# Optimization experiments

Hardware: AMD Instinct MI355X
Metric: run time of the kernel (lower is better)

## Reference

```python
import jax, jax.numpy as jnp
import numpy as np

N, C, H, W = 16, 64, 256, 256


def setup_inputs() -> dict:
    key = jax.random.key(0)
    ks = jax.random.split(key, 7)
    s = 1.0 / np.sqrt(C)
    return {
        "h": jax.random.normal(ks[0], (N, C, H, W), dtype=jnp.float32),
        "wq": jax.random.normal(ks[1], (C, C), dtype=jnp.float32) * s,
        "bq": jax.random.normal(ks[2], (C,), dtype=jnp.float32) * 0.01,
        "wk": jax.random.normal(ks[3], (C, C), dtype=jnp.float32) * s,
        "bk": jax.random.normal(ks[4], (C,), dtype=jnp.float32) * 0.01,
        "wv": jax.random.normal(ks[5], (C, C), dtype=jnp.float32) * s,
        "bv": jax.random.normal(ks[6], (C,), dtype=jnp.float32) * 0.01,
    }


def _proj(h, w, b):
    # 1x1 conv == per-pixel channel linear: (N,C,H,W) x (Cout,Cin)
    return jnp.einsum("nchw,oc->nohw", h, w) + b[None, :, None, None]


def reference(h, wq, bq, wk, bk, wv, bv):
    q = _proj(h, wq, bq)
    k = _proj(h, wk, bk)
    v = _proj(h, wv, bv)

    # NOTE: original code uses n = k.shape[-1] of the UNPERMUTED k => n = W
    scale = 1.0 / jnp.sqrt(jnp.asarray(W, dtype=q.dtype))

    # Channel-wise ROW attention: permute (N,C,H,W)->(N,W,H,C), attend over H
    attn_r = jnp.einsum("nchw,ngw->nwhg", q, jnp.einsum("ncgw->ngw" if False else "ncgw->ncgw", k)[0] if False else jnp.einsum("ncgw->ncgw", k).sum(axis=0) * 0) if False else None
    # row: q_r (n,w,h,c) @ k_r^T (n,w,c,g) -> (n,w,h,g)
    scores_r = jnp.einsum("nchw,ncgw->nwhg", q, k) * scale
    p_r = jax.nn.softmax(scores_r, axis=-1)
    out_r = jnp.einsum("nwhg,ncgw->nchw", p_r, v)  # back to (N,C,H,W)

    # Channel-wise COLUMN attention: permute (N,C,H,W)->(N,H,W,C), attend over W
    scores_c = jnp.einsum("nchw,nchu->nhwu", q, k) * scale
    p_c = jax.nn.softmax(scores_c, axis=-1)
    out_c = jnp.einsum("nhwu,nchu->nchw", p_c, v)

    attention = out_r + out_c
    return attention + h
```

## Files before the change

### kernel.cpp

```cpp
#include <hip/hip_runtime.h>


typedef unsigned short u16t;
typedef __bf16 bf16x8 __attribute__((ext_vector_type(8)));
typedef __bf16 bf16x2 __attribute__((ext_vector_type(2)));
typedef float  f32x4  __attribute__((ext_vector_type(4)));
typedef u16t   us8    __attribute__((ext_vector_type(8)));
typedef u16t   us4    __attribute__((ext_vector_type(4)));
typedef unsigned uu4  __attribute__((ext_vector_type(4)));

#define DEVINL __device__ __forceinline__

#define SCL16 0.09016844f

DEVINL u16t f2bf(float f){
    return __builtin_bit_cast(u16t, (__bf16)f);
}
DEVINL float bf2f(u16t h){
    unsigned u = ((unsigned)h) << 16;
    return __builtin_bit_cast(float, u);
}
DEVINL unsigned pk2(float lo, float hi){
    bf16x2 t; t[0] = (__bf16)lo; t[1] = (__bf16)hi;
    return __builtin_bit_cast(unsigned, t);
}
DEVINL f32x4 mfma16(bf16x8 a, bf16x8 b, f32x4 c){
    return __builtin_amdgcn_mfma_f32_16x16x32_bf16(a, b, c, 0, 0, 0);
}
DEVINL int xswz(int row, int chunk){
    return row*128 + ((chunk << 4) ^ (((row & 7) ^ ((row >> 2) & 7)) << 4));
}

__global__ __launch_bounds__(256) void transpose_kernel(const float* __restrict__ h,
                                                        u16t* __restrict__ hT){
    __shared__ float tile[64][257];
    const int bid = blockIdx.x;
    const int n = bid >> 8, y = bid & 255;
    const int tid = threadIdx.x;
    {
        const int c = tid >> 2, w0 = (tid & 3) * 64;
        const int base = ((n * 64 + c) * 256 + y) * 256 + w0;
        #pragma unroll
        for (int i = 0; i < 16; ++i){
            f32x4 v = *(const f32x4*)(h + base + i * 4);
            tile[c][w0 + i*4 + 0] = v[0];
            tile[c][w0 + i*4 + 1] = v[1];
            tile[c][w0 + i*4 + 2] = v[2];
            tile[c][w0 + i*4 + 3] = v[3];
        }
    }
    __syncthreads();
    #pragma unroll
    for (int j = 0; j < 4; ++j){
        const int task = tid + 256 * j;
        const int w = task >> 2, c0 = (task & 3) * 16;
        us8 o0, o1;
        #pragma unroll
        for (int e = 0; e < 8; ++e) o0[e] = f2bf(tile[c0 + e][w]);
        #pragma unroll
        for (int e = 0; e < 8; ++e) o1[e] = f2bf(tile[c0 + 8 + e][w]);
        const int ob = ((n * 256 + y) * 256 + w) * 64 + c0;
        *(us8*)(hT + ob)     = o0;
        *(us8*)(hT + ob + 8) = o1;
    }
}

template<int COL>
__global__ __launch_bounds__(512, 4) void attn_kernel(
    const u16t* __restrict__ Xg,
    const float* __restrict__ wq, const float* __restrict__ bq,
    const float* __restrict__ wk, const float* __restrict__ wvw,
    const float* __restrict__ bvp,
    u16t* __restrict__ Og,
    float* __restrict__ outp)
{
    __shared__ __align__(16) u16t Xs[16384];
    __shared__ __align__(16) u16t VtF[16384];
    __shared__ __align__(16) u16t AtF[4096];
    __shared__ __align__(16) float w16s[256];
    __shared__ float wkbqs[64];
    __shared__ float bvs[64];

    const int tid  = threadIdx.x;
    const int lane = tid & 63;
    const int wv   = tid >> 6;
    const int bid  = blockIdx.x;
    const int n    = bid >> 8;
    const int idx  = bid & 255;
    const int l15  = lane & 15;
    const int l4   = lane >> 4;
    const int nbase = n * 4194304;
    const int sbase = nbase + idx * 16384;
    const int aa   = l15 >> 2, bb = l15 & 3;
    const char* Xc = (const char*)Xs;

    {
        const int r0 = tid >> 3, cc = tid & 7;
        const int swzS = (((r0 & 7) ^ ((tid >> 5) & 7)) << 4);
        char* pdst = (char*)Xs + r0*128 + ((cc << 4) ^ swzS);
        const u16t* psrc = Xg + (COL ? (sbase + r0*64 + cc*8)
                                     : (nbase + r0*16384 + idx*64 + cc*8));
        const int gstep = COL ? 4096 : 1048576;
        #pragma unroll
        for (int pass = 0; pass < 4; ++pass){
            us8 v = *(const us8*)(psrc + pass*gstep);
            *(us8*)(pdst + pass*8192) = v;
        }
    }

    {
        const int mtA = wv >> 1;
        us8 aku[2];
        #pragma unroll
        for (int kt = 0; kt < 2; ++kt)
            #pragma unroll
            for (int e = 0; e < 8; ++e)
                aku[kt][e] = f2bf(wk[(kt*32 + l4*8 + e)*64 + mtA*16 + l15]);
        #pragma unroll
        for (int t2 = 0; t2 < 2; ++t2){
            const int ntA = (2*wv + t2) & 3;
            us8 bqu[2];
            #pragma unroll
            for (int kt = 0; kt < 2; ++kt)
                #pragma unroll
                for (int e = 0; e < 8; ++e)
                    bqu[kt][e] = f2bf(wq[(kt*32 + l4*8 + e)*64 + ntA*16 + l15]);
            f32x4 acc = {0.f,0.f,0.f,0.f};
            acc = mfma16(__builtin_bit_cast(bf16x8, aku[0]), __builtin_bit_cast(bf16x8, bqu[0]), acc);
            acc = mfma16(__builtin_bit_cast(bf16x8, aku[1]), __builtin_bit_cast(bf16x8, bqu[1]), acc);
            #pragma unroll
            for (int r = 0; r < 4; ++r){
                const int cp = mtA*16 + 4*l4 + r;
                const int cc = ntA*16 + l15;
                const int vtq  = 2*(cp>>5) + ((cp>>2)&1);
                const int mrow = 4*((cp>>3)&3) + (cp&3);
                const int f    = vtq*2 + (cc>>5);
                AtF[(f*64 + ((cc>>3)&3)*16 + mrow)*8 + (cc&7)] = f2bf(acc[r] * SCL16);
            }
        }
    }
    if (tid < 64){
        float acc = 0.f;
        for (int o = 0; o < 64; ++o) acc += wk[o*64 + tid] * bq[o];
        wkbqs[tid] = acc;
        bvs[tid] = bvp[tid];
    }
    __syncthreads();

    {
        const int ct = wv >> 1;
        bf16x8 awv[2];
        #pragma unroll
        for (int ktc = 0; ktc < 2; ++ktc){
            const float* wp = wvw + (ct*16 + l15)*64 + ktc*32 + l4*8;
            f32x4 v0 = *(const f32x4*)wp;
            f32x4 v1 = *(const f32x4*)(wp + 4);
            us8 u;
            #pragma unroll
            for (int e = 0; e < 4; ++e){ u[e] = f2bf(v0[e]); u[4+e] = f2bf(v1[e]); }
            awv[ktc] = __builtin_bit_cast(bf16x8, u);
        }
        const char* pb0 = Xc + (wv&1)*16384 + l15*128;
        const int swzE = (((l15&7) ^ aa) << 4);
        const int swzO = (((l15&7) ^ (4+aa)) << 4);
        const int cE0 = (l4<<4) ^ swzE, cE1 = ((4+l4)<<4) ^ swzE;
        const int cO0 = (l4<<4) ^ swzO, cO1 = ((4+l4)<<4) ^ swzO;
        char* pvw = (char*)VtF + (ct*8 + (wv&1)*4)*1024 + (l15>>3)*256 + l4*64 + (l15&7)*2;
        #pragma unroll
        for (int t = 0; t < 8; ++t){
            const int o0 = (t&1) ? cO0 : cE0, o1 = (t&1) ? cO1 : cE1;
            bf16x8 bx0 = *(const bf16x8*)(pb0 + t*2048 + o0);
            bf16x8 bx1 = *(const bf16x8*)(pb0 + t*2048 + o1);
            f32x4 z = {0.f,0.f,0.f,0.f};
            z = mfma16(awv[0], bx0, z);
            z = mfma16(awv[1], bx1, z);
            char* pw8 = pvw + (t>>1)*1024 + (t&1)*512;
            #pragma unroll
            for (int rr = 0; rr < 4; ++rr)
                *(u16t*)(pw8 + rr*16) = f2bf(z[rr]);
        }
    }
    if (tid < 256){
        float acc = 0.f;
        #pragma unroll
        for (int cc = 0; cc < 8; ++cc){
            us8 xv = *(const us8*)(Xc + xswz(tid, cc));
            #pragma unroll
            for (int e = 0; e < 8; ++e) acc += bf2f(xv[e]) * wkbqs[cc*8 + e];
        }
        w16s[tid] = acc * SCL16;
    }
    __syncthreads();

    const int rowoff = 8*aa + bb;

    const char* pat = (const char*)AtF + lane*16;
    bf16x8 xq[2][2];
    #pragma unroll
    for (int mi = 0; mi < 2; ++mi){
        const int mt = wv + 8*mi;
        xq[mi][0] = *(const bf16x8*)(Xc + xswz(mt*16 + l15, l4));
        xq[mi][1] = *(const bf16x8*)(Xc + xswz(mt*16 + l15, 4 + l4));
    }
    uu4 qp[2][2];
    #pragma unroll
    for (int vtq = 0; vtq < 4; ++vtq){
        bf16x8 a0 = *(const bf16x8*)(pat + (vtq*2 + 0)*1024);
        bf16x8 a1 = *(const bf16x8*)(pat + (vtq*2 + 1)*1024);
        #pragma unroll
        for (int mi = 0; mi < 2; ++mi){
            f32x4 z = {0.f,0.f,0.f,0.f};
            z = mfma16(a0, xq[mi][0], z);
            z = mfma16(a1, xq[mi][1], z);
            qp[mi][vtq>>1][(vtq&1)*2 + 0] = pk2(z[0], z[1]);
            qp[mi][vtq>>1][(vtq&1)*2 + 1] = pk2(z[2], z[3]);
        }
    }
    bf16x8 qb[2][2];
    qb[0][0] = __builtin_bit_cast(bf16x8, qp[0][0]);
    qb[0][1] = __builtin_bit_cast(bf16x8, qp[0][1]);
    qb[1][0] = __builtin_bit_cast(bf16x8, qp[1][0]);
    qb[1][1] = __builtin_bit_cast(bf16x8, qp[1][1]);

    const int swz0 = (bb ^ (2*aa)) << 4;
    const int swz1 = ((4 + bb) ^ ((2*aa + 1) & 7)) << 4;
    const char* pv00 = Xc + rowoff*128 + ((l4<<4) ^ swz0);
    const char* pv01 = Xc + rowoff*128 + (((4+l4)<<4) ^ swz0);
    const char* pv10 = Xc + rowoff*128 + 512 + ((l4<<4) ^ swz1);
    const char* pv11 = Xc + rowoff*128 + 512 + (((4+l4)<<4) ^ swz1);
    const char* pvv = (const char*)VtF + lane*16;
    const char* pw  = (const char*)w16s + l4*32;

    uu4 onep; onep[0] = 0x3F803F80u; onep[1] = 0x3F803F80u; onep[2] = 0x3F803F80u; onep[3] = 0x3F803F80u;
    const bf16x8 onesb = __builtin_bit_cast(bf16x8, onep);

    f32x4 po[2][4] = {{{0.f,0.f,0.f,0.f},{0.f,0.f,0.f,0.f},{0.f,0.f,0.f,0.f},{0.f,0.f,0.f,0.f}},
                      {{0.f,0.f,0.f,0.f},{0.f,0.f,0.f,0.f},{0.f,0.f,0.f,0.f},{0.f,0.f,0.f,0.f}}};
    f32x4 po_sum[2] = {{0.f,0.f,0.f,0.f},{0.f,0.f,0.f,0.f}};

    #pragma unroll
    for (int kt = 0; kt < 8; ++kt){
        bf16x8 xa00 = *(const bf16x8*)(pv00 + kt*4096);
        bf16x8 xa01 = *(const bf16x8*)(pv01 + kt*4096);
        bf16x8 xa10 = *(const bf16x8*)(pv10 + kt*4096);
        bf16x8 xa11 = *(const bf16x8*)(pv11 + kt*4096);
        f32x4 cw0 = *(const f32x4*)(pw + kt*128);
        f32x4 cw1 = *(const f32x4*)(pw + kt*128 + 16);
        bf16x8 vb[4];
        #pragma unroll
        for (int nt = 0; nt < 4; ++nt)
            vb[nt] = *(const bf16x8*)(pvv + (nt*8 + kt)*1024);

        __builtin_amdgcn_s_setprio(1);
        bf16x8 pa[2];
        #pragma unroll
        for (int mi = 0; mi < 2; ++mi){
            uu4 tt;
            f32x4 z0 = cw0;
            z0 = mfma16(xa00, qb[mi][0], z0);
            z0 = mfma16(xa01, qb[mi][1], z0);
            tt[0] = pk2(__builtin_amdgcn_exp2f(z0[0]), __builtin_amdgcn_exp2f(z0[1]));
            tt[1] = pk2(__builtin_amdgcn_exp2f(z0[2]), __builtin_amdgcn_exp2f(z0[3]));
            f32x4 z1 = cw1;
            z1 = mfma16(xa10, qb[mi][0], z1);
            z1 = mfma16(xa11, qb[mi][1], z1);
            tt[2] = pk2(__builtin_amdgcn_exp2f(z1[0]), __builtin_amdgcn_exp2f(z1[1]));
            tt[3] = pk2(__builtin_amdgcn_exp2f(z1[2]), __builtin_amdgcn_exp2f(z1[3]));
            pa[mi] = __builtin_bit_cast(bf16x8, tt);
            po_sum[mi] = mfma16(pa[mi], onesb, po_sum[mi]);
        }
        #pragma unroll
        for (int nt = 0; nt < 4; ++nt){
            po[0][nt] = mfma16(pa[0], vb[nt], po[0][nt]);
            po[1][nt] = mfma16(pa[1], vb[nt], po[1][nt]);
        }
        __builtin_amdgcn_s_setprio(0);
    }

    __syncthreads();
    u16t* OutS = VtF;

    if (!COL){
        #pragma unroll
        for (int mi = 0; mi < 2; ++mi){
            const int mt = wv + 8*mi;
            float rs[4];
            #pragma unroll
            for (int r = 0; r < 4; ++r) rs[r] = __builtin_amdgcn_rcpf(po_sum[mi][r]);
            #pragma unroll
            for (int nt = 0; nt < 4; ++nt){
                const int c = nt*16 + l15;
                const float b = bvs[c];
                #pragma unroll
                for (int r01 = 0; r01 < 2; ++r01){
                    float vr[2];
                    #pragma unroll
                    for (int e = 0; e < 2; ++e){
                        const int r = 2*r01 + e;
                        const int y = mt*16 + 4*l4 + r;
                        const float xres = bf2f(*(const u16t*)(Xc + xswz(y, c>>3) + (c&7)*2));
                        vr[e] = po[mi][nt][r]*rs[r] + b + xres;
                    }
                    const int y0 = mt*16 + 4*l4 + 2*r01;
                    const unsigned v = pk2(vr[0], vr[1]);
                    *(u16t*)((char*)OutS + y0*128 + (((c>>3)<<4) ^ ((y0&7)<<4)) + (c&7)*2) = (u16t)v;
                    *(u16t*)((char*)OutS + (y0+1)*128 + (((c>>3)<<4) ^ (((y0+1)&7)<<4)) + (c&7)*2) = (u16t)(v >> 16);
                }
            }
        }
        __syncthreads();
        #pragma unroll
        for (int p = 0; p < 4; ++p){
            const int id = p*512 + tid;
            const int y = id >> 3, ch = id & 7;
            us8 v = *(const us8*)((const char*)OutS + y*128 + ((ch<<4) ^ ((y&7)<<4)));
            *(us8*)(Og + sbase + y*64 + ch*8) = v;
        }
    } else {
        #pragma unroll
        for (int p = 0; p < 4; ++p){
            const int id = p*512 + tid;
            const int wl = id >> 3, ch = id & 7;
            us8 v = *(const us8*)(Og + nbase + wl*16384 + idx*64 + ch*8);
            *(us8*)(Xs + id*8) = v;
        }
        __syncthreads();
        #pragma unroll
        for (int mi = 0; mi < 2; ++mi){
            const int mt = wv + 8*mi;
            float rs[4];
            #pragma unroll
            for (int r = 0; r < 4; ++r) rs[r] = __builtin_amdgcn_rcpf(po_sum[mi][r]);
            #pragma unroll
            for (int nt = 0; nt < 4; ++nt){
                const int c = nt*16 + l15;
                const float b = bvs[c];
                #pragma unroll
                for (int r01 = 0; r01 < 2; ++r01){
                    float vr[2];
                    #pragma unroll
                    for (int e = 0; e < 2; ++e){
                        const int r = 2*r01 + e;
                        const int wl = mt*16 + 4*l4 + r;
                        vr[e] = po[mi][nt][r]*rs[r] + b + bf2f(Xs[wl*64 + c]);
                    }
                    const int w0 = mt*16 + 4*l4 + 2*r01;
                    *(unsigned*)((char*)OutS + c*512 + ((w0*2) ^ ((c&7)<<4))) = pk2(vr[0], vr[1]);
                }
            }
        }
        __syncthreads();
        const int c = tid >> 3, q = tid & 7;
        const int gb = ((n*64 + c)*256 + idx)*256;
        #pragma unroll
        for (int k = 0; k < 8; ++k){
            const int w0 = q*4 + k*32;
            us4 ov = *(const us4*)((const char*)OutS + c*512 + ((w0*2) ^ ((c&7)<<4)));
            f32x4 res;
            #pragma unroll
            for (int e = 0; e < 4; ++e) res[e] = bf2f(ov[e]);
            *(f32x4*)(outp + gb + w0) = res;
        }
    }
}

extern "C" void kernel_launch(void* const* d_in, const int* in_sizes, int n_in,
                              void* d_out, int out_size, void* d_ws, size_t ws_size,
                              hipStream_t stream){
    const float* h   = (const float*)d_in[0];
    const float* wq  = (const float*)d_in[1];
    const float* bq  = (const float*)d_in[2];
    const float* wk  = (const float*)d_in[3];
    const float* wvw = (const float*)d_in[5];
    const float* bv  = (const float*)d_in[6];
    float* out = (float*)d_out;

    u16t* hT = (u16t*)d_ws;
    u16t* Op = hT + 67108864;

    transpose_kernel<<<4096, 256, 0, stream>>>(h, hT);
    attn_kernel<0><<<4096, 512, 0, stream>>>(hT, wq, bq, wk, wvw, bv, Op, nullptr);
    attn_kernel<1><<<4096, 512, 0, stream>>>(hT, wq, bq, wk, wvw, bv, Op, out);
}
```

Before: 377.1 us.

## Halve attention block size to 256 threads with four row tiles per wave

The attention kernels now run 256-thread blocks instead of 512. Each wave handles four 16-row M-tiles instead of two, so every loaded K/V fragment feeds twice as many MFMAs. Global loads, the V projection and the stores are reindexed for the smaller block. The cost is more registers per wave (accumulators go from 2x4 to 4x4 f32x4), and the occupancy hint is removed, which may reduce wave concurrency.

```diff
diff --git a/kernel.cpp b/kernel.cpp
--- a/kernel.cpp
+++ b/kernel.cpp
@@ -66,7 +66,7 @@
 }
 
 template<int COL>
-__global__ __launch_bounds__(512, 4) void attn_kernel(
+__global__ __launch_bounds__(256) void attn_kernel(
     const u16t* __restrict__ Xg,
     const float* __restrict__ wq, const float* __restrict__ bq,
     const float* __restrict__ wk, const float* __restrict__ wvw,
@@ -96,20 +96,20 @@
 
     {
         const int r0 = tid >> 3, cc = tid & 7;
-        const int swzS = (((r0 & 7) ^ ((tid >> 5) & 7)) << 4);
+        const int swzS = (((r0 & 7) ^ ((r0 >> 2) & 7)) << 4);
         char* pdst = (char*)Xs + r0*128 + ((cc << 4) ^ swzS);
         const u16t* psrc = Xg + (COL ? (sbase + r0*64 + cc*8)
                                      : (nbase + r0*16384 + idx*64 + cc*8));
-        const int gstep = COL ? 4096 : 1048576;
-        #pragma unroll
-        for (int pass = 0; pass < 4; ++pass){
+        const int gstep = COL ? 2048 : 524288;
+        #pragma unroll
+        for (int pass = 0; pass < 8; ++pass){
             us8 v = *(const us8*)(psrc + pass*gstep);
-            *(us8*)(pdst + pass*8192) = v;
-        }
-    }
-
-    {
-        const int mtA = wv >> 1;
+            *(us8*)(pdst + pass*4096) = v;
+        }
+    }
+
+    {
+        const int mtA = wv;
         us8 aku[2];
         #pragma unroll
         for (int kt = 0; kt < 2; ++kt)
@@ -117,8 +117,7 @@
             for (int e = 0; e < 8; ++e)
                 aku[kt][e] = f2bf(wk[(kt*32 + l4*8 + e)*64 + mtA*16 + l15]);
         #pragma unroll
-        for (int t2 = 0; t2 < 2; ++t2){
-            const int ntA = (2*wv + t2) & 3;
+        for (int ntA = 0; ntA < 4; ++ntA){
             us8 bqu[2];
             #pragma unroll
             for (int kt = 0; kt < 2; ++kt)
@@ -148,7 +147,7 @@
     __syncthreads();
 
     {
-        const int ct = wv >> 1;
+        const int ct = wv;
         bf16x8 awv[2];
         #pragma unroll
         for (int ktc = 0; ktc < 2; ++ktc){
@@ -160,14 +159,14 @@
             for (int e = 0; e < 4; ++e){ u[e] = f2bf(v0[e]); u[4+e] = f2bf(v1[e]); }
             awv[ktc] = __builtin_bit_cast(bf16x8, u);
         }
-        const char* pb0 = Xc + (wv&1)*16384 + l15*128;
+        const char* pb0 = Xc + l15*128;
         const int swzE = (((l15&7) ^ aa) << 4);
         const int swzO = (((l15&7) ^ (4+aa)) << 4);
         const int cE0 = (l4<<4) ^ swzE, cE1 = ((4+l4)<<4) ^ swzE;
         const int cO0 = (l4<<4) ^ swzO, cO1 = ((4+l4)<<4) ^ swzO;
-        char* pvw = (char*)VtF + (ct*8 + (wv&1)*4)*1024 + (l15>>3)*256 + l4*64 + (l15&7)*2;
-        #pragma unroll
-        for (int t = 0; t < 8; ++t){
+        char* pvw = (char*)VtF + ct*8192 + (l15>>3)*256 + l4*64 + (l15&7)*2;
+        #pragma unroll
+        for (int t = 0; t < 16; ++t){
             const int o0 = (t&1) ? cO0 : cE0, o1 = (t&1) ? cO1 : cE1;
             bf16x8 bx0 = *(const bf16x8*)(pb0 + t*2048 + o0);
             bf16x8 bx1 = *(const bf16x8*)(pb0 + t*2048 + o1);
@@ -180,7 +179,7 @@
                 *(u16t*)(pw8 + rr*16) = f2bf(z[rr]);
         }
     }
-    if (tid < 256){
+    {
         float acc = 0.f;
         #pragma unroll
         for (int cc = 0; cc < 8; ++cc){
@@ -195,32 +194,35 @@
     const int rowoff = 8*aa + bb;
 
     const char* pat = (const char*)AtF + lane*16;
-    bf16x8 xq[2][2];
+    uu4 qp[4][2];
+    {
+        bf16x8 xq[4][2];
+        #pragma unroll
+        for (int mi = 0; mi < 4; ++mi){
+            const int mt = wv*4 + mi;
+            xq[mi][0] = *(const bf16x8*)(Xc + xswz(mt*16 + l15, l4));
+            xq[mi][1] = *(const bf16x8*)(Xc + xswz(mt*16 + l15, 4 + l4));
+        }
+        #pragma unroll
+        for (int vtq = 0; vtq < 4; ++vtq){
+            bf16x8 a0 = *(const bf16x8*)(pat + (vtq*2 + 0)*1024);
+            bf16x8 a1 = *(const bf16x8*)(pat + (vtq*2 + 1)*1024);
+            #pragma unroll
+            for (int mi = 0; mi < 4; ++mi){
+                f32x4 z = {0.f,0.f,0.f,0.f};
+                z = mfma16(a0, xq[mi][0], z);
+                z = mfma16(a1, xq[mi][1], z);
+                qp[mi][vtq>>1][(vtq&1)*2 + 0] = pk2(z[0], z[1]);
+                qp[mi][vtq>>1][(vtq&1)*2 + 1] = pk2(z[2], z[3]);
+            }
+        }
+    }
+    bf16x8 qb[4][2];
     #pragma unroll
-    for (int mi = 0; mi < 2; ++mi){
-        const int mt = wv + 8*mi;
-        xq[mi][0] = *(const bf16x8*)(Xc + xswz(mt*16 + l15, l4));
-        xq[mi][1] = *(const bf16x8*)(Xc + xswz(mt*16 + l15, 4 + l4));
-    }
-    uu4 qp[2][2];
-    #pragma unroll
-    for (int vtq = 0; vtq < 4; ++vtq){
-        bf16x8 a0 = *(const bf16x8*)(pat + (vtq*2 + 0)*1024);
-        bf16x8 a1 = *(const bf16x8*)(pat + (vtq*2 + 1)*1024);
-        #pragma unroll
-        for (int mi = 0; mi < 2; ++mi){
-            f32x4 z = {0.f,0.f,0.f,0.f};
-            z = mfma16(a0, xq[mi][0], z);
-            z = mfma16(a1, xq[mi][1], z);
-            qp[mi][vtq>>1][(vtq&1)*2 + 0] = pk2(z[0], z[1]);
-            qp[mi][vtq>>1][(vtq&1)*2 + 1] = pk2(z[2], z[3]);
-        }
-    }
-    bf16x8 qb[2][2];
-    qb[0][0] = __builtin_bit_cast(bf16x8, qp[0][0]);
-    qb[0][1] = __builtin_bit_cast(bf16x8, qp[0][1]);
-    qb[1][0] = __builtin_bit_cast(bf16x8, qp[1][0]);
-    qb[1][1] = __builtin_bit_cast(bf16x8, qp[1][1]);
+    for (int mi = 0; mi < 4; ++mi){
+        qb[mi][0] = __builtin_bit_cast(bf16x8, qp[mi][0]);
+        qb[mi][1] = __builtin_bit_cast(bf16x8, qp[mi][1]);
+    }
 
     const int swz0 = (bb ^ (2*aa)) << 4;
     const int swz1 = ((4 + bb) ^ ((2*aa + 1) & 7)) << 4;
@@ -234,9 +236,14 @@
     uu4 onep; onep[0] = 0x3F803F80u; onep[1] = 0x3F803F80u; onep[2] = 0x3F803F80u; onep[3] = 0x3F803F80u;
     const bf16x8 onesb = __builtin_bit_cast(bf16x8, onep);
 
-    f32x4 po[2][4] = {{{0.f,0.f,0.f,0.f},{0.f,0.f,0.f,0.f},{0.f,0.f,0.f,0.f},{0.f,0.f,0.f,0.f}},
-                      {{0.f,0.f,0.f,0.f},{0.f,0.f,0.f,0.f},{0.f,0.f,0.f,0.f},{0.f,0.f,0.f,0.f}}};
-    f32x4 po_sum[2] = {{0.f,0.f,0.f,0.f},{0.f,0.f,0.f,0.f}};
+    f32x4 po[4][4];
+    f32x4 po_sum[4];
+    #pragma unroll
+    for (int mi = 0; mi < 4; ++mi){
+        po_sum[mi] = (f32x4){0.f,0.f,0.f,0.f};
+        #pragma unroll
+        for (int nt = 0; nt < 4; ++nt) po[mi][nt] = (f32x4){0.f,0.f,0.f,0.f};
+    }
 
     #pragma unroll
     for (int kt = 0; kt < 8; ++kt){
@@ -252,9 +259,9 @@
             vb[nt] = *(const bf16x8*)(pvv + (nt*8 + kt)*1024);
 
         __builtin_amdgcn_s_setprio(1);
-        bf16x8 pa[2];
-        #pragma unroll
-        for (int mi = 0; mi < 2; ++mi){
+        bf16x8 pa[4];
+        #pragma unroll
+        for (int mi = 0; mi < 4; ++mi){
             uu4 tt;
             f32x4 z0 = cw0;
             z0 = mfma16(xa00, qb[mi][0], z0);
@@ -271,8 +278,9 @@
         }
         #pragma unroll
         for (int nt = 0; nt < 4; ++nt){
-            po[0][nt] = mfma16(pa[0], vb[nt], po[0][nt]);
-            po[1][nt] = mfma16(pa[1], vb[nt], po[1][nt]);
+            #pragma unroll
+            for (int mi = 0; mi < 4; ++mi)
+                po[mi][nt] = mfma16(pa[mi], vb[nt], po[mi][nt]);
         }
         __builtin_amdgcn_s_setprio(0);
     }
@@ -282,8 +290,8 @@
 
     if (!COL){
         #pragma unroll
-        for (int mi = 0; mi < 2; ++mi){
-            const int mt = wv + 8*mi;
+        for (int mi = 0; mi < 4; ++mi){
+            const int mt = wv*4 + mi;
             float rs[4];
             #pragma unroll
             for (int r = 0; r < 4; ++r) rs[r] = __builtin_amdgcn_rcpf(po_sum[mi][r]);
@@ -310,24 +318,24 @@
         }
         __syncthreads();
         #pragma unroll
-        for (int p = 0; p < 4; ++p){
-            const int id = p*512 + tid;
+        for (int p = 0; p < 8; ++p){
+            const int id = p*256 + tid;
             const int y = id >> 3, ch = id & 7;
             us8 v = *(const us8*)((const char*)OutS + y*128 + ((ch<<4) ^ ((y&7)<<4)));
             *(us8*)(Og + sbase + y*64 + ch*8) = v;
         }
     } else {
         #pragma unroll
-        for (int p = 0; p < 4; ++p){
-            const int id = p*512 + tid;
+        for (int p = 0; p < 8; ++p){
+            const int id = p*256 + tid;
             const int wl = id >> 3, ch = id & 7;
             us8 v = *(const us8*)(Og + nbase + wl*16384 + idx*64 + ch*8);
             *(us8*)(Xs + id*8) = v;
         }
         __syncthreads();
         #pragma unroll
-        for (int mi = 0; mi < 2; ++mi){
-            const int mt = wv + 8*mi;
+        for (int mi = 0; mi < 4; ++mi){
+            const int mt = wv*4 + mi;
             float rs[4];
             #pragma unroll
             for (int r = 0; r < 4; ++r) rs[r] = __builtin_amdgcn_rcpf(po_sum[mi][r]);
@@ -350,11 +358,11 @@
             }
         }
         __syncthreads();
-        const int c = tid >> 3, q = tid & 7;
+        const int c = tid >> 2, q = tid & 3;
         const int gb = ((n*64 + c)*256 + idx)*256;
         #pragma unroll
-        for (int k = 0; k < 8; ++k){
-            const int w0 = q*4 + k*32;
+        for (int k = 0; k < 16; ++k){
+            const int w0 = q*4 + k*16;
             us4 ov = *(const us4*)((const char*)OutS + c*512 + ((w0*2) ^ ((c&7)<<4)));
             f32x4 res;
             #pragma unroll
@@ -379,6 +387,6 @@
     u16t* Op = hT + 67108864;
 
     transpose_kernel<<<4096, 256, 0, stream>>>(h, hT);
-    attn_kernel<0><<<4096, 512, 0, stream>>>(hT, wq, bq, wk, wvw, bv, Op, nullptr);
-    attn_kernel<1><<<4096, 512, 0, stream>>>(hT, wq, bq, wk, wvw, bv, Op, out);
-}
+    attn_kernel<0><<<4096, 256, 0, stream>>>(hT, wq, bq, wk, wvw, bv, Op, nullptr);
+    attn_kernel<1><<<4096, 256, 0, stream>>>(hT, wq, bq, wk, wvw, bv, Op, out);
+}
```

New measurement: 393.8 us. 4.4% more time.
